# Optimization experiments

Hardware: AMD Instinct MI355X
Metric: run time of the kernel (lower is better)

The kernel has to match this reference:

```python
import jax, jax.numpy as jnp
import numpy as np

N_DOC, SEQ, HID, HEADS = 4, 1024, 768, 12
NE, NM, NP = 48, 4, 1000
L, EMB, BLK, GHID = 97, 768, 64, 500
NEDGE_R = 800


def setup_inputs() -> dict:
    key = jax.random.key(0)
    ks = jax.random.split(key, 24)
    s = 0.02
    att = jax.random.uniform(ks[1], (N_DOC, HEADS, SEQ, SEQ), jnp.float32)
    inp = {
        "sequence_output": jax.random.normal(ks[0], (N_DOC, SEQ, HID), jnp.float32),
        "attention": att / att.sum(-1, keepdims=True),
        "mention_starts": jax.random.randint(ks[2], (N_DOC, NE, NM), 0, SEQ - 2),
        "mention_mask": jnp.ones((N_DOC, NE, NM), jnp.bool_),
        "hts": jax.random.randint(ks[3], (N_DOC, NP, 2), 0, NE),
        "label_emb": jax.random.normal(ks[4], (L, EMB), jnp.float32),
        "gat_W0": jax.random.normal(ks[5], (EMB, 2 * GHID), jnp.float32) * s,
        "gat_al0": jax.random.normal(ks[6], (2, GHID), jnp.float32) * s,
        "gat_ar0": jax.random.normal(ks[7], (2, GHID), jnp.float32) * s,
        "gat_b0": jnp.zeros((2 * GHID,), jnp.float32),
        "gat_W1": jax.random.normal(ks[8], (2 * GHID, EMB), jnp.float32) * s,
        "gat_al1": jax.random.normal(ks[9], (1, EMB), jnp.float32) * s,
        "gat_ar1": jax.random.normal(ks[10], (1, EMB), jnp.float32) * s,
        "gat_b1": jnp.zeros((EMB,), jnp.float32),
        "edge_src": jnp.concatenate([jax.random.randint(ks[11], (NEDGE_R,), 0, L), jnp.arange(L)]),
        "edge_dst": jnp.concatenate([jax.random.randint(ks[12], (NEDGE_R,), 0, L), jnp.arange(L)]),
        "head_W": jax.random.normal(ks[13], (2 * HID, EMB), jnp.float32) * s,
        "head_b": jnp.zeros((EMB,), jnp.float32),
        "tail_W": jax.random.normal(ks[14], (2 * HID, EMB), jnp.float32) * s,
        "tail_b": jnp.zeros((EMB,), jnp.float32),
        "ln_g": jnp.ones((L,), jnp.float32),
        "ln_b": jnp.zeros((L,), jnp.float32),
        "lin2_W": jax.random.normal(ks[15], (2 * L, L), jnp.float32) * s,
        "lin2_b": jnp.zeros((L,), jnp.float32),
        "bil_W": jax.random.normal(ks[16], (EMB * BLK + L, L), jnp.float32) * s,
        "bil_b": jnp.zeros((L,), jnp.float32),
    }
    return inp


def gat_layer(x, W, al, ar, b, src, dst, n_nodes):
    # DGL-style GATConv: per-head linear, additive attention, softmax over incoming edges.
    heads, out_dim = al.shape
    feat = (x @ W).reshape(-1, heads, out_dim)          # [N, H, D]
    el = (feat * al[None]).sum(-1)                      # [N, H]
    er = (feat * ar[None]).sum(-1)
    e = jax.nn.leaky_relu(el[src] + er[dst], 0.2)       # [E, H]
    emax = jax.ops.segment_max(e, dst, num_segments=n_nodes)
    w = jnp.exp(e - emax[dst])
    den = jax.ops.segment_sum(w, dst, num_segments=n_nodes)
    alpha = w / (den[dst] + 1e-9)
    out = jax.ops.segment_sum(alpha[:, :, None] * feat[src], dst, num_segments=n_nodes)
    return out + b.reshape(heads, out_dim)              # [N, H, D]


def reference(sequence_output, attention, mention_starts, mention_mask, hts, label_emb,
              gat_W0, gat_al0, gat_ar0, gat_b0, gat_W1, gat_al1, gat_ar1, gat_b1,
              edge_src, edge_dst, head_W, head_b, tail_W, tail_b,
              ln_g, ln_b, lin2_W, lin2_b, bil_W, bil_b):
    n, c, d = sequence_output.shape
    nl = label_emb.shape[0]
    OFFSET = 1  # bert-style cls offset
    pos = mention_starts + OFFSET                               # [n, E, M], all < c
    bi = jnp.arange(n)[:, None, None]
    m_emb = sequence_output[bi, pos]                            # [n, E, M, d]
    m_att = attention[bi, :, pos]                               # [n, E, M, h, c]
    mf = mention_mask.astype(sequence_output.dtype)
    cnt = mf.sum(2)                                             # [n, E]
    lse = jax.nn.logsumexp(jnp.where(mention_mask[..., None], m_emb, -1e30), axis=2)
    ent_emb = jnp.where(cnt[..., None] > 0, lse, 0.0)           # [n, E, d]
    ent_att = (m_att * mf[..., None, None]).sum(2) / (cnt[..., None, None] + 1e-9)  # [n, E, h, c]
    bi2 = jnp.arange(n)[:, None]
    hidx, tidx = hts[..., 0], hts[..., 1]
    hs = ent_emb[bi2, hidx]                                     # [n, P, d]
    ts = ent_emb[bi2, tidx]
    ht = (ent_att[bi2, hidx] * ent_att[bi2, tidx]).mean(2)      # [n, P, c]
    ht = ht / (ht.sum(-1, keepdims=True) + 1e-5)
    rs = jnp.einsum('npc,ncd->npd', ht, sequence_output)        # [n, P, d]
    hs, ts, rs = hs.reshape(-1, d), ts.reshape(-1, d), rs.reshape(-1, d)
    # GAT over the label co-occurrence graph
    h0 = jax.nn.elu(gat_layer(label_emb, gat_W0, gat_al0, gat_ar0, gat_b0, edge_src, edge_dst, nl))
    h0 = h0.reshape(nl, -1)                                     # concat 2 heads -> [L, 1000]
    lab = gat_layer(h0, gat_W1, gat_al1, gat_ar1, gat_b1, edge_src, edge_dst, nl).mean(1)  # [L, emb]
    def lnorm(x):
        mu = x.mean(-1, keepdims=True)
        v = ((x - mu) ** 2).mean(-1, keepdims=True)
        return (x - mu) / jnp.sqrt(v + 1e-5) * ln_g + ln_b
    hsl = lnorm(hs @ lab.T)
    tsl = lnorm(ts @ lab.T)
    logits_lab = jnp.concatenate([hsl, tsl], 1) @ lin2_W + lin2_b   # [N, L]
    h2 = jnp.tanh(jnp.concatenate([hs, rs], 1) @ head_W + head_b)   # [N, emb]
    t2 = jnp.tanh(jnp.concatenate([ts, rs], 1) @ tail_W + tail_b)
    emb = h2.shape[1]
    b1 = h2.reshape(-1, emb // BLK, BLK)
    b2 = t2.reshape(-1, emb // BLK, BLK)
    bl = (b1[:, :, :, None] * b2[:, :, None, :]).reshape(-1, emb * BLK)  # [N, emb*blk]
    logits = jnp.concatenate([bl, logits_lab], 1) @ bil_W + bil_b        # [N, L]
    return logits
```

## Files before the change

kernel.cpp:

```cpp
#include <hip/hip_runtime.h>
#include <hip/hip_bf16.h>
#include <math.h>

#define NDOC 4
#define SEQL 1024
#define HIDD 768
#define NHEADS 12
#define NEENT 48
#define NMEN 4
#define NPAIR 1000
#define NLAB 97
#define GHID 500
#define NEDGE 897
#define NROW (NDOC*NPAIR)

#define KBIL 49152
#define KSTEPS_MAIN 1536
#define KSTEPS_TOT 1540
#define NPAD 128
#define NPOUT 112
#define NCHUNK 12
#define NMT64 63

#define PB_WPREP 3080
#define PB_SEQ   1536
#define PB_EMB   192
#define PB_ATT   2304

typedef __attribute__((ext_vector_type(8))) short short8v;
typedef __attribute__((ext_vector_type(4))) short short4v;
typedef __attribute__((ext_vector_type(4))) float f32x4;
typedef _Float16 half8v __attribute__((ext_vector_type(8)));
typedef unsigned int uint4v __attribute__((ext_vector_type(4)));

__device__ __forceinline__ unsigned short f2bfbits(float x) {
    return __builtin_bit_cast(unsigned short, __float2bfloat16(x));
}

__device__ __forceinline__ float block_reduce_sum(float v, float* red) {
    int tid = threadIdx.x;
    red[tid] = v;
    __syncthreads();
    for (int s = blockDim.x >> 1; s > 0; s >>= 1) {
        if (tid < s) red[tid] += red[tid + s];
        __syncthreads();
    }
    float r = red[0];
    __syncthreads();
    return r;
}

__device__ __forceinline__ float block_reduce_max(float v, float* red) {
    int tid = threadIdx.x;
    red[tid] = v;
    __syncthreads();
    for (int s = blockDim.x >> 1; s > 0; s >>= 1) {
        if (tid < s) red[tid] = fmaxf(red[tid], red[tid + s]);
        __syncthreads();
    }
    float r = red[0];
    __syncthreads();
    return r;
}

__global__ void __launch_bounds__(256) k_prep_all(
    const float* __restrict__ bil_W, _Float16* __restrict__ Wb,
    const float* __restrict__ seq, __hip_bfloat16* __restrict__ seqb,
    const int* __restrict__ mstarts, float* __restrict__ ent_emb,
    const float* __restrict__ att, float* __restrict__ ent_att)
{
    int bid = blockIdx.x;
    if (bid < PB_WPREP) {
        int t = bid * 256 + threadIdx.x;
        int lane = t & 63;
        int nt = (t >> 6) & 7;
        int kt = t >> 9;
        int col = nt * 16 + (lane & 15);
        int kbase = kt * 32 + ((lane >> 4) << 3);
        half8v v;
        #pragma unroll
        for (int e = 0; e < 8; ++e) {
            int k = kbase + e;
            float x = (col < NLAB && k < (KBIL + NLAB)) ? bil_W[(size_t)k * NLAB + col] : 0.f;
            v[e] = (_Float16)x;
        }
        ((half8v*)Wb)[t] = v;
    } else if (bid < PB_WPREP + PB_SEQ) {
        int t = (bid - PB_WPREP) * 256 + threadIdx.x;
        int lane = t & 63;
        int rest = t >> 6;
        int dt = rest % 48; rest /= 48;
        int kt = rest % 32;
        int doc = rest / 32;
        int d = dt * 16 + (lane & 15);
        int kbase = kt * 32 + ((lane >> 4) << 3);
        short8v v;
        #pragma unroll
        for (int e = 0; e < 8; ++e)
            v[e] = (short)f2bfbits(seq[((size_t)doc * SEQL + kbase + e) * HIDD + d]);
        ((short8v*)seqb)[t] = v;
    } else if (bid < PB_WPREP + PB_SEQ + PB_EMB) {
        int be = bid - (PB_WPREP + PB_SEQ);
        int b = be / NEENT;
        int pos[NMEN];
        #pragma unroll
        for (int m = 0; m < NMEN; ++m) pos[m] = mstarts[be * NMEN + m] + 1;
        for (int d = threadIdx.x; d < HIDD; d += 256) {
            float v0 = seq[((size_t)b * SEQL + pos[0]) * HIDD + d];
            float v1 = seq[((size_t)b * SEQL + pos[1]) * HIDD + d];
            float v2 = seq[((size_t)b * SEQL + pos[2]) * HIDD + d];
            float v3 = seq[((size_t)b * SEQL + pos[3]) * HIDD + d];
            float mx = fmaxf(fmaxf(v0, v1), fmaxf(v2, v3));
            float s = expf(v0 - mx) + expf(v1 - mx) + expf(v2 - mx) + expf(v3 - mx);
            ent_emb[(size_t)be * HIDD + d] = mx + logf(s);
        }
    } else {
        int idx = bid - (PB_WPREP + PB_SEQ + PB_EMB);
        int h = idx % NHEADS;
        int be = idx / NHEADS;
        int b = be / NEENT;
        int pos[NMEN];
        #pragma unroll
        for (int m = 0; m < NMEN; ++m) pos[m] = mstarts[be * NMEN + m] + 1;
        const float* abase = att + ((size_t)b * NHEADS + h) * SEQL * SEQL;
        for (int s = threadIdx.x; s < SEQL; s += 256) {
            float acc = 0.f;
            #pragma unroll
            for (int m = 0; m < NMEN; ++m) acc += abase[(size_t)pos[m] * SEQL + s];
            ent_att[(size_t)idx * SEQL + s] = acc * 0.25f;
        }
    }
}

__global__ void __launch_bounds__(256) k_prep2(
    const float* __restrict__ head_W, __hip_bfloat16* __restrict__ Whb,
    const float* __restrict__ tail_W, __hip_bfloat16* __restrict__ Wtb,
    const float* __restrict__ ent_emb, __hip_bfloat16* __restrict__ emb_bf)
{
    int bid = blockIdx.x;
    if (bid < 1152) {
        const float* W = bid < 576 ? head_W : tail_W;
        __hip_bfloat16* Wf = bid < 576 ? Whb : Wtb;
        int t = (bid % 576) * 256 + threadIdx.x;
        int lane = t & 63;
        int ntile = (t >> 6) % 48;
        int kt = t / (48 * 64);
        int col = ntile * 16 + (lane & 15);
        int kbase = kt * 32 + ((lane >> 4) << 3);
        short8v v;
        #pragma unroll
        for (int e = 0; e < 8; ++e)
            v[e] = (short)f2bfbits(W[(size_t)(kbase + e) * HIDD + col]);
        ((short8v*)Wf)[t] = v;
    } else {
        int t = (bid - 1152) * 256 + threadIdx.x;
        if (t >= NDOC * NEENT * HIDD / 8) return;
        const float4* p = (const float4*)(ent_emb + (size_t)t * 8);
        float4 a = p[0], b = p[1];
        short8v v;
        v[0] = (short)f2bfbits(a.x); v[1] = (short)f2bfbits(a.y);
        v[2] = (short)f2bfbits(a.z); v[3] = (short)f2bfbits(a.w);
        v[4] = (short)f2bfbits(b.x); v[5] = (short)f2bfbits(b.y);
        v[6] = (short)f2bfbits(b.z); v[7] = (short)f2bfbits(b.w);
        ((short8v*)emb_bf)[t] = v;
    }
}

template<int K, int N>
__global__ void __launch_bounds__(256) k_gemm2(
    const float* __restrict__ A, const float* __restrict__ W, float* __restrict__ C)
{
    const int JT = (N + 255) / 256;
    int n  = blockIdx.x / JT;
    int jt = blockIdx.x % JT;
    int j = jt * 256 + threadIdx.x;
    if (j >= N) return;
    const float* a = A + (size_t)n * K;
    float acc0 = 0.f, acc1 = 0.f, acc2 = 0.f, acc3 = 0.f;
    float acc4 = 0.f, acc5 = 0.f, acc6 = 0.f, acc7 = 0.f;
    for (int k = 0; k < K; k += 8) {
        acc0 += a[k + 0] * W[(size_t)(k + 0) * N + j];
        acc1 += a[k + 1] * W[(size_t)(k + 1) * N + j];
        acc2 += a[k + 2] * W[(size_t)(k + 2) * N + j];
        acc3 += a[k + 3] * W[(size_t)(k + 3) * N + j];
        acc4 += a[k + 4] * W[(size_t)(k + 4) * N + j];
        acc5 += a[k + 5] * W[(size_t)(k + 5) * N + j];
        acc6 += a[k + 6] * W[(size_t)(k + 6) * N + j];
        acc7 += a[k + 7] * W[(size_t)(k + 7) * N + j];
    }
    C[(size_t)n * N + j] = ((acc0 + acc1) + (acc2 + acc3)) + ((acc4 + acc5) + (acc6 + acc7));
}

template<int NH, int OD>
__global__ void k_eler(const float* __restrict__ feat, const float* __restrict__ al,
                       const float* __restrict__ ar, float* __restrict__ el,
                       float* __restrict__ er)
{
    __shared__ float red[256];
    int n = blockIdx.x;
    for (int h = 0; h < NH; ++h) {
        float a = 0.f, b = 0.f;
        for (int k = threadIdx.x; k < OD; k += blockDim.x) {
            float f = feat[(size_t)n * NH * OD + h * OD + k];
            a += f * al[h * OD + k];
            b += f * ar[h * OD + k];
        }
        float sa = block_reduce_sum(a, red);
        float sb = block_reduce_sum(b, red);
        if (threadIdx.x == 0) { el[n * NH + h] = sa; er[n * NH + h] = sb; }
    }
}

template<int NH, int OD, int QN, int DO_ELU>
__global__ void k_gat_agg(const float* __restrict__ feat,
                          const float* __restrict__ el, const float* __restrict__ er,
                          const int* __restrict__ esrc, const int* __restrict__ edst,
                          const float* __restrict__ bias, float* __restrict__ out)
{
    __shared__ float red[256];
    __shared__ int ss[NEDGE];
    __shared__ int dd[NEDGE];
    int n = blockIdx.x;
    for (int t = threadIdx.x; t < NEDGE; t += blockDim.x) { ss[t] = esrc[t]; dd[t] = edst[t]; }
    __syncthreads();
    float ern[NH], emax[NH], den[NH];
    #pragma unroll
    for (int h = 0; h < NH; ++h) ern[h] = er[n * NH + h];
    #pragma unroll
    for (int h = 0; h < NH; ++h) {
        float mx = -1e30f;
        for (int t = threadIdx.x; t < NEDGE; t += blockDim.x) {
            if (dd[t] == n) {
                float x = el[ss[t] * NH + h] + ern[h];
                x = x > 0.f ? x : 0.2f * x;
                mx = fmaxf(mx, x);
            }
        }
        emax[h] = block_reduce_max(mx, red);
        float sm = 0.f;
        for (int t = threadIdx.x; t < NEDGE; t += blockDim.x) {
            if (dd[t] == n) {
                float x = el[ss[t] * NH + h] + ern[h];
                x = x > 0.f ? x : 0.2f * x;
                sm += expf(x - emax[h]);
            }
        }
        den[h] = block_reduce_sum(sm, red);
    }
    float acc[QN];
    #pragma unroll
    for (int q = 0; q < QN; ++q) acc[q] = 0.f;
    for (int t = 0; t < NEDGE; ++t) {
        if (dd[t] != n) continue;
        int s = ss[t];
        float alpha[NH];
        #pragma unroll
        for (int h = 0; h < NH; ++h) {
            float x = el[s * NH + h] + ern[h];
            x = x > 0.f ? x : 0.2f * x;
            alpha[h] = expf(x - emax[h]) / (den[h] + 1e-9f);
        }
        #pragma unroll
        for (int q = 0; q < QN; ++q) {
            int idx = threadIdx.x + q * 256;
            if (idx < NH * OD) {
                int h = idx / OD;
                acc[q] += alpha[h] * feat[(size_t)s * NH * OD + idx];
            }
        }
    }
    #pragma unroll
    for (int q = 0; q < QN; ++q) {
        int idx = threadIdx.x + q * 256;
        if (idx < NH * OD) {
            float v = acc[q] + bias[idx];
            out[(size_t)n * NH * OD + idx] = DO_ELU ? (v > 0.f ? v : expm1f(v)) : v;
        }
    }
}

__global__ void k_labtrans(const float* __restrict__ lab, float* __restrict__ labT)
{
    int t = blockIdx.x * 256 + threadIdx.x;
    if (t >= NLAB * HIDD) return;
    int l = t / HIDD, d = t - l * HIDD;
    labT[d * NLAB + l] = lab[t];
}

__global__ void __launch_bounds__(128) k_ent_lab(
    const float* __restrict__ ent_emb, const float* __restrict__ labT,
    const float* __restrict__ ln_g, const float* __restrict__ ln_b,
    float* __restrict__ EL)
{
    __shared__ float e[HIDD];
    __shared__ float red[128];
    int be = blockIdx.x;
    for (int k = threadIdx.x; k < HIDD; k += 128) e[k] = ent_emb[(size_t)be * HIDD + k];
    __syncthreads();
    int l = threadIdx.x;
    float a = 0.f;
    if (l < NLAB)
        for (int k = 0; k < HIDD; ++k) a += e[k] * labT[k * NLAB + l];
    float v = (l < NLAB) ? a : 0.f;
    float s  = block_reduce_sum(v, red);
    float s2 = block_reduce_sum(v * v, red);
    const float invL = 1.0f / NLAB;
    float mu = s * invL;
    float var = s2 * invL - mu * mu;
    float is = 1.0f / sqrtf(var + 1e-5f);
    if (l < NLAB) EL[be * NLAB + l] = (a - mu) * is * ln_g[l] + ln_b[l];
}

__global__ void __launch_bounds__(128) k_lin2(
    const float* __restrict__ EL, const int* __restrict__ hts,
    const float* __restrict__ lin2_W, const float* __restrict__ lin2_b,
    _Float16* __restrict__ llhf)
{
    __shared__ float sh[NLAB], st[NLAB];
    int n = blockIdx.x;
    int b = n / NPAIR;
    int hi = hts[n * 2], ti = hts[n * 2 + 1];
    int l = threadIdx.x;
    if (l < NLAB) {
        sh[l] = EL[(b * NEENT + hi) * NLAB + l];
        st[l] = EL[(b * NEENT + ti) * NLAB + l];
    }
    __syncthreads();
    float a = 0.f;
    if (l < NLAB) {
        a = lin2_b[l];
        for (int q = 0; q < NLAB; ++q)
            a += sh[q] * lin2_W[q * NLAB + l] + st[q] * lin2_W[(NLAB + q) * NLAB + l];
    }
    llhf[(size_t)n * NPAD + l] = (_Float16)(l < NLAB ? a : 0.f);
}

__global__ void __launch_bounds__(256) k_ht(
    const float* __restrict__ ent_att, const int* __restrict__ hts,
    __hip_bfloat16* __restrict__ HTb)
{
    __shared__ float red[256];
    int n = blockIdx.x;
    n = (n & 7) * 500 + (n >> 3);
    int b = n / NPAIR;
    int hi = hts[n * 2], ti = hts[n * 2 + 1];
    const float* ha = ent_att + ((size_t)(b * NEENT + hi)) * NHEADS * SEQL;
    const float* ta = ent_att + ((size_t)(b * NEENT + ti)) * NHEADS * SEQL;
    int s0 = threadIdx.x * 4;
    float4 acc = {0.f, 0.f, 0.f, 0.f};
    #pragma unroll
    for (int h = 0; h < NHEADS; ++h) {
        float4 a = *(const float4*)&ha[h * SEQL + s0];
        float4 t = *(const float4*)&ta[h * SEQL + s0];
        acc.x += a.x * t.x; acc.y += a.y * t.y; acc.z += a.z * t.z; acc.w += a.w * t.w;
    }
    const float inv12 = 1.0f / NHEADS;
    acc.x *= inv12; acc.y *= inv12; acc.z *= inv12; acc.w *= inv12;
    float Z = block_reduce_sum(acc.x + acc.y + acc.z + acc.w, red);
    float scale = 1.0f / (Z + 1e-5f);
    int nloc = n % NPAIR;
    short4v v;
    v.x = (short)f2bfbits(acc.x * scale);
    v.y = (short)f2bfbits(acc.y * scale);
    v.z = (short)f2bfbits(acc.z * scale);
    v.w = (short)f2bfbits(acc.w * scale);
    *(short4v*)&HTb[((size_t)b * 1024 + nloc) * SEQL + s0] = v;
}

__global__ void __launch_bounds__(256) k_rs_mfma(
    const __hip_bfloat16* __restrict__ HTb, const __hip_bfloat16* __restrict__ seqb,
    __hip_bfloat16* __restrict__ rsb)
{
    int b = blockIdx.x;
    int wg = (b & 7) * 96 + (b >> 3);
    int doc = wg / 192;
    int rem = wg % 192;
    int mtile = rem / 6, ngrp = rem % 6;
    int tid = threadIdx.x, wave = tid >> 6, lane = tid & 63;
    int mh = wave & 1, ng = wave >> 1;
    int lr = lane & 15, lg = lane >> 4;
    int rowl = mtile * 32 + mh * 16 + lr;
    const short8v* av = (const short8v*)(HTb + (((size_t)doc * 1024 + rowl) * SEQL));
    const short8v* bv = (const short8v*)seqb;
    int dtbase = ngrp * 8 + ng * 4;
    f32x4 acc[4];
    #pragma unroll
    for (int nt = 0; nt < 4; ++nt) acc[nt] = f32x4{0.f, 0.f, 0.f, 0.f};
    for (int kt = 0; kt < 32; ++kt) {
        short8v af = av[kt * 4 + lg];
        const short8v* wp = bv + ((((size_t)doc * 32 + kt) * 48 + dtbase) * 64 + lane);
        #pragma unroll
        for (int nt = 0; nt < 4; ++nt)
            acc[nt] = __builtin_amdgcn_mfma_f32_16x16x32_bf16(af, wp[nt * 64], acc[nt], 0, 0, 0);
    }
    #pragma unroll
    for (int nt = 0; nt < 4; ++nt) {
        int d = ngrp * 128 + ng * 64 + nt * 16 + lr;
        #pragma unroll
        for (int r = 0; r < 4; ++r) {
            int nloc = mtile * 32 + mh * 16 + lg * 4 + r;
            if (nloc < NPAIR)
                rsb[((size_t)(doc * NPAIR + nloc)) * HIDD + d] = __float2bfloat16(acc[nt][r]);
        }
    }
}

__global__ void __launch_bounds__(256) k_ht2_mfma(
    const __hip_bfloat16* __restrict__ emb_bf, const __hip_bfloat16* __restrict__ rsb,
    const int* __restrict__ hts,
    const __hip_bfloat16* __restrict__ Whb, const __hip_bfloat16* __restrict__ Wtb,
    const float* __restrict__ head_b, const float* __restrict__ tail_b,
    float* __restrict__ h2, float* __restrict__ t2)
{
    int bid = blockIdx.x;
    int which = bid >= (NMT64 * 6) ? 1 : 0;
    int rem = bid - which * (NMT64 * 6);
    int mtile = rem / 6, ngrp = rem % 6;
    int tid = threadIdx.x, wave = tid >> 6, lane = tid & 63;
    int ng = wave & 1, mp = wave >> 1;
    int lr = lane & 15, lg = lane >> 4;
    int na = mtile * 64 + mp * 32 + lr;
    int nb = na + 16;
    int nac = na < NROW ? na : NROW - 1;
    int nbc = nb < NROW ? nb : NROW - 1;
    int ba = nac / NPAIR, bb = nbc / NPAIR;
    int enta = hts[nac * 2 + which];
    int entb = hts[nbc * 2 + which];
    const short8v* embrow_a = (const short8v*)emb_bf + (size_t)(ba * NEENT + enta) * 96;
    const short8v* embrow_b = (const short8v*)emb_bf + (size_t)(bb * NEENT + entb) * 96;
    const short8v* rsrow_a  = (const short8v*)rsb + (size_t)nac * 96;
    const short8v* rsrow_b  = (const short8v*)rsb + (size_t)nbc * 96;
    const short8v* wv = (const short8v*)(which ? Wtb : Whb);
    const float* bias = which ? tail_b : head_b;
    float* out = which ? t2 : h2;
    f32x4 acc[2][4];
    #pragma unroll
    for (int m = 0; m < 2; ++m)
        #pragma unroll
        for (int nt = 0; nt < 4; ++nt) acc[m][nt] = f32x4{0.f, 0.f, 0.f, 0.f};
    int ntbase = ngrp * 8 + ng * 4;
    for (int kt = 0; kt < 24; ++kt) {
        short8v afa = embrow_a[kt * 4 + lg];
        short8v afb = embrow_b[kt * 4 + lg];
        const short8v* wp = wv + ((kt * 48 + ntbase) * 64 + lane);
        #pragma unroll
        for (int nt = 0; nt < 4; ++nt) {
            short8v bf = wp[nt * 64];
            acc[0][nt] = __builtin_amdgcn_mfma_f32_16x16x32_bf16(afa, bf, acc[0][nt], 0, 0, 0);
            acc[1][nt] = __builtin_amdgcn_mfma_f32_16x16x32_bf16(afb, bf, acc[1][nt], 0, 0, 0);
        }
    }
    for (int kt = 24; kt < 48; ++kt) {
        short8v afa = rsrow_a[(kt - 24) * 4 + lg];
        short8v afb = rsrow_b[(kt - 24) * 4 + lg];
        const short8v* wp = wv + ((kt * 48 + ntbase) * 64 + lane);
        #pragma unroll
        for (int nt = 0; nt < 4; ++nt) {
            short8v bf = wp[nt * 64];
            acc[0][nt] = __builtin_amdgcn_mfma_f32_16x16x32_bf16(afa, bf, acc[0][nt], 0, 0, 0);
            acc[1][nt] = __builtin_amdgcn_mfma_f32_16x16x32_bf16(afb, bf, acc[1][nt], 0, 0, 0);
        }
    }
    #pragma unroll
    for (int m = 0; m < 2; ++m) {
        #pragma unroll
        for (int nt = 0; nt < 4; ++nt) {
            int col = ngrp * 128 + ng * 64 + nt * 16 + lr;
            float bj = bias[col];
            #pragma unroll
            for (int r = 0; r < 4; ++r) {
                int n2 = mtile * 64 + mp * 32 + m * 16 + lg * 4 + r;
                if (n2 < NROW)
                    out[(size_t)n2 * HIDD + col] = tanhf(acc[m][nt][r] + bj);
            }
        }
    }
}

__global__ void __launch_bounds__(256) k_bilin_mfma(
    const float* __restrict__ h2, const float* __restrict__ t2,
    const _Float16* __restrict__ llhf, const _Float16* __restrict__ Wb,
    float* __restrict__ pout)
{
    __shared__ unsigned int hs2[64 * 68];
    __shared__ _Float16 ts[64 * 72];
    int bid = blockIdx.x;
    int c = bid % NCHUNK;
    int mtile = bid / NCHUNK;
    int n0 = mtile * 64;
    int tid = threadIdx.x;
    int wave = tid >> 6, lane = tid & 63;
    int ng = wave & 1, mp = wave >> 1;
    int lr = lane & 15;
    int lg = lane >> 4;
    int koff = lg << 3;
    int rowa = mp * 32 + lr;
    int rowb = rowa + 16;
    f32x4 acc[2][4];
    #pragma unroll
    for (int m = 0; m < 2; ++m)
        #pragma unroll
        for (int nt = 0; nt < 4; ++nt) acc[m][nt] = f32x4{0.f, 0.f, 0.f, 0.f};

    const half8v* wbv = (const half8v*)Wb;

    for (int idx = tid; idx < 4096; idx += 256) {
        int r = idx >> 6, cc = idx & 63;
        float hv = h2[(size_t)(n0 + r) * HIDD + c * 64 + cc];
        float tv = t2[(size_t)(n0 + r) * HIDD + c * 64 + cc];
        unsigned short hb = __builtin_bit_cast(unsigned short, (_Float16)hv);
        hs2[r * 68 + cc] = ((unsigned int)hb << 16) | hb;
        ts[r * 72 + cc] = (_Float16)tv;
    }
    __syncthreads();
    for (int j0 = 0; j0 < 64; j0 += 32) {
        half8v tva = *(const half8v*)&ts[rowa * 72 + j0 + koff];
        half8v tvb = *(const half8v*)&ts[rowb * 72 + j0 + koff];
        int ktbase = c * 128 + (j0 >> 5);
        #pragma unroll 4
        for (int i = 0; i < 64; ++i) {
            unsigned int ha = hs2[rowa * 68 + i];
            unsigned int hb = hs2[rowb * 68 + i];
            half8v afa = __builtin_bit_cast(half8v, uint4v{ha, ha, ha, ha}) * tva;
            half8v afb = __builtin_bit_cast(half8v, uint4v{hb, hb, hb, hb}) * tvb;
            int kt = ktbase + i * 2;
            const half8v* wp = wbv + ((kt * 8 + ng * 4) * 64 + lane);
            #pragma unroll
            for (int nt = 0; nt < 4; ++nt) {
                half8v bf = wp[nt * 64];
                acc[0][nt] = __builtin_amdgcn_mfma_f32_16x16x32_f16(afa, bf, acc[0][nt], 0, 0, 0);
                acc[1][nt] = __builtin_amdgcn_mfma_f32_16x16x32_f16(afb, bf, acc[1][nt], 0, 0, 0);
            }
        }
    }
    if (c == NCHUNK - 1) {
        const half8v* lv = (const half8v*)llhf;
        #pragma unroll
        for (int tt = 0; tt < 4; ++tt) {
            half8v afa = lv[(size_t)(n0 + rowa) * 16 + tt * 4 + lg];
            half8v afb = lv[(size_t)(n0 + rowb) * 16 + tt * 4 + lg];
            int kt = KSTEPS_MAIN + tt;
            const half8v* wp = wbv + ((kt * 8 + ng * 4) * 64 + lane);
            #pragma unroll
            for (int nt = 0; nt < 4; ++nt) {
                half8v bf = wp[nt * 64];
                acc[0][nt] = __builtin_amdgcn_mfma_f32_16x16x32_f16(afa, bf, acc[0][nt], 0, 0, 0);
                acc[1][nt] = __builtin_amdgcn_mfma_f32_16x16x32_f16(afb, bf, acc[1][nt], 0, 0, 0);
            }
        }
    }
    #pragma unroll
    for (int m = 0; m < 2; ++m) {
        #pragma unroll
        for (int nt = 0; nt < 4; ++nt) {
            int col = ng * 64 + nt * 16 + lr;
            if (col < NPOUT) {
                #pragma unroll
                for (int r = 0; r < 4; ++r) {
                    int rown = n0 + mp * 32 + m * 16 + lg * 4 + r;
                    if (rown < NROW)
                        pout[((size_t)c * NROW + rown) * NPOUT + col] = acc[m][nt][r];
                }
            }
        }
    }
}

__global__ void k_bilin_reduce(const float* __restrict__ pout,
                               const float* __restrict__ bil_b,
                               float* __restrict__ out)
{
    int t = blockIdx.x * 256 + threadIdx.x;
    if (t >= NROW * NLAB) return;
    int n = t / NLAB, l = t - n * NLAB;
    float a = bil_b[l];
    #pragma unroll
    for (int q = 0; q < NCHUNK; ++q) a += pout[((size_t)q * NROW + n) * NPOUT + l];
    out[t] = a;
}

extern "C" void kernel_launch(void* const* d_in, const int* in_sizes, int n_in,
                              void* d_out, int out_size, void* d_ws, size_t ws_size,
                              hipStream_t stream)
{
    (void)in_sizes; (void)n_in; (void)out_size; (void)ws_size;
    const float* seq       = (const float*)d_in[0];
    const float* att       = (const float*)d_in[1];
    const int*   mstarts   = (const int*)d_in[2];
    const int*   hts       = (const int*)d_in[4];
    const float* label_emb = (const float*)d_in[5];
    const float* gat_W0    = (const float*)d_in[6];
    const float* gat_al0   = (const float*)d_in[7];
    const float* gat_ar0   = (const float*)d_in[8];
    const float* gat_b0    = (const float*)d_in[9];
    const float* gat_W1    = (const float*)d_in[10];
    const float* gat_al1   = (const float*)d_in[11];
    const float* gat_ar1   = (const float*)d_in[12];
    const float* gat_b1    = (const float*)d_in[13];
    const int*   esrc      = (const int*)d_in[14];
    const int*   edst      = (const int*)d_in[15];
    const float* head_W    = (const float*)d_in[16];
    const float* head_b    = (const float*)d_in[17];
    const float* tail_W    = (const float*)d_in[18];
    const float* tail_b    = (const float*)d_in[19];
    const float* ln_g      = (const float*)d_in[20];
    const float* ln_b      = (const float*)d_in[21];
    const float* lin2_W    = (const float*)d_in[22];
    const float* lin2_b    = (const float*)d_in[23];
    const float* bil_W     = (const float*)d_in[24];
    const float* bil_b     = (const float*)d_in[25];
    float* out = (float*)d_out;
    float* ws  = (float*)d_ws;

    float* ent_emb    = ws;
    float* ent_att    = ws + 147456;
    float* rs_region  = ws + 2506752;
    float* h2         = ws + 5578752;
    float* t2         = ws + 8650752;
    float* EL         = ws + 11722752;
    float* labT       = ws + 11741376;
    float* feat0      = ws + 12110752;
    float* el0        = ws + 12207752;
    float* er0        = ws + 12207952;
    float* h0         = ws + 12208152;
    float* feat1      = ws + 12305152;
    float* el1        = ws + 12379648;
    float* er1        = ws + 12379752;
    float* lab        = ws + 12379856;
    _Float16* llhf    = (_Float16*)(ws + 12454352);
    _Float16* Wb      = (_Float16*)(ws + 12710352);
    __hip_bfloat16* Whb    = (__hip_bfloat16*)(ws + 147456);
    __hip_bfloat16* Wtb    = (__hip_bfloat16*)(ws + 147456 + 589824);
    __hip_bfloat16* emb_bf = (__hip_bfloat16*)(ws + 147456 + 1179648);
    float* pout = ws + 147456;
    __hip_bfloat16* HTb  = (__hip_bfloat16*)h2;
    __hip_bfloat16* seqb = (__hip_bfloat16*)t2;
    __hip_bfloat16* rsb  = (__hip_bfloat16*)rs_region;

    k_prep_all<<<PB_WPREP + PB_SEQ + PB_EMB + PB_ATT, 256, 0, stream>>>(
        bil_W, Wb, seq, seqb, mstarts, ent_emb, att, ent_att);

    k_gemm2<768, 1000><<<NLAB * 4, 256, 0, stream>>>(label_emb, gat_W0, feat0);
    k_eler<2, 500><<<NLAB, 256, 0, stream>>>(feat0, gat_al0, gat_ar0, el0, er0);
    k_gat_agg<2, 500, 4, 1><<<NLAB, 256, 0, stream>>>(feat0, el0, er0, esrc, edst, gat_b0, h0);
    k_gemm2<1000, 768><<<NLAB * 3, 256, 0, stream>>>(h0, gat_W1, feat1);
    k_eler<1, 768><<<NLAB, 256, 0, stream>>>(feat1, gat_al1, gat_ar1, el1, er1);
    k_gat_agg<1, 768, 3, 0><<<NLAB, 256, 0, stream>>>(feat1, el1, er1, esrc, edst, gat_b1, lab);

    k_labtrans<<<(NLAB * HIDD + 255) / 256, 256, 0, stream>>>(lab, labT);
    k_ent_lab<<<NDOC * NEENT, 128, 0, stream>>>(ent_emb, labT, ln_g, ln_b, EL);
    k_lin2<<<NROW, 128, 0, stream>>>(EL, hts, lin2_W, lin2_b, llhf);

    k_ht<<<NROW, 256, 0, stream>>>(ent_att, hts, HTb);

    k_prep2<<<1224, 256, 0, stream>>>(head_W, Whb, tail_W, Wtb, ent_emb, emb_bf);

    k_rs_mfma<<<768, 256, 0, stream>>>(HTb, seqb, rsb);

    k_ht2_mfma<<<2 * NMT64 * 6, 256, 0, stream>>>(emb_bf, rsb, hts, Whb, Wtb, head_b, tail_b, h2, t2);

    k_bilin_mfma<<<NMT64 * NCHUNK, 256, 0, stream>>>(h2, t2, llhf, Wb, pout);
    k_bilin_reduce<<<(NROW * NLAB + 255) / 256, 256, 0, stream>>>(pout, bil_b, out);
}
```

Baseline: 470.4 us.

## Fuse prep kernels, prefetch MFMA operands, split bilinear chunks finer

Folds the first GAT GEMM and the head/tail weight conversion into the big prep kernel. It merges the label transpose into the GAT aggregation and the entity bf16 conversion into k_ht, which removes several launches. The rs and ht2 MFMA loops now load the next k-step's operands one iteration ahead (software prefetch), and the bilinear kernel splits each chunk into two j-halves (NCHUNK 24), giving more blocks and a smaller LDS footprint. The workspace is re-laid out so buffers no longer alias, and the cost is a larger pout and twice as many partials to reduce.

```diff
diff --git a/kernel.cpp b/kernel.cpp
--- a/kernel.cpp
+++ b/kernel.cpp
@@ -19,13 +19,16 @@
 #define KSTEPS_TOT 1540
 #define NPAD 128
 #define NPOUT 112
-#define NCHUNK 12
+#define NCHUNK 24
 #define NMT64 63
 
+#define PB_G0    388
 #define PB_WPREP 3080
 #define PB_SEQ   1536
 #define PB_EMB   192
 #define PB_ATT   2304
+#define PB_WHT   1152
+#define PB_TOT   (PB_G0+PB_WPREP+PB_SEQ+PB_EMB+PB_ATT+PB_WHT)
 
 typedef __attribute__((ext_vector_type(8))) short short8v;
 typedef __attribute__((ext_vector_type(4))) short short4v;
@@ -64,12 +67,37 @@
 }
 
 __global__ void __launch_bounds__(256) k_prep_all(
+    const float* __restrict__ label_emb, const float* __restrict__ gat_W0,
+    float* __restrict__ feat0,
     const float* __restrict__ bil_W, _Float16* __restrict__ Wb,
     const float* __restrict__ seq, __hip_bfloat16* __restrict__ seqb,
     const int* __restrict__ mstarts, float* __restrict__ ent_emb,
-    const float* __restrict__ att, float* __restrict__ ent_att)
+    const float* __restrict__ att, float* __restrict__ ent_att,
+    const float* __restrict__ head_W, __hip_bfloat16* __restrict__ Whb,
+    const float* __restrict__ tail_W, __hip_bfloat16* __restrict__ Wtb)
 {
     int bid = blockIdx.x;
+    if (bid < PB_G0) {
+        int n = bid >> 2, jt = bid & 3;
+        int j = jt * 256 + threadIdx.x;
+        if (j < 1000) {
+            const float* a = label_emb + (size_t)n * 768;
+            float a0=0.f,a1=0.f,a2=0.f,a3=0.f,a4=0.f,a5=0.f,a6=0.f,a7=0.f;
+            for (int k = 0; k < 768; k += 8) {
+                a0 += a[k+0] * gat_W0[(size_t)(k+0)*1000 + j];
+                a1 += a[k+1] * gat_W0[(size_t)(k+1)*1000 + j];
+                a2 += a[k+2] * gat_W0[(size_t)(k+2)*1000 + j];
+                a3 += a[k+3] * gat_W0[(size_t)(k+3)*1000 + j];
+                a4 += a[k+4] * gat_W0[(size_t)(k+4)*1000 + j];
+                a5 += a[k+5] * gat_W0[(size_t)(k+5)*1000 + j];
+                a6 += a[k+6] * gat_W0[(size_t)(k+6)*1000 + j];
+                a7 += a[k+7] * gat_W0[(size_t)(k+7)*1000 + j];
+            }
+            feat0[(size_t)n*1000 + j] = ((a0+a1)+(a2+a3))+((a4+a5)+(a6+a7));
+        }
+        return;
+    }
+    bid -= PB_G0;
     if (bid < PB_WPREP) {
         int t = bid * 256 + threadIdx.x;
         int lane = t & 63;
@@ -85,8 +113,11 @@
             v[e] = (_Float16)x;
         }
         ((half8v*)Wb)[t] = v;
-    } else if (bid < PB_WPREP + PB_SEQ) {
-        int t = (bid - PB_WPREP) * 256 + threadIdx.x;
+        return;
+    }
+    bid -= PB_WPREP;
+    if (bid < PB_SEQ) {
+        int t = bid * 256 + threadIdx.x;
         int lane = t & 63;
         int rest = t >> 6;
         int dt = rest % 48; rest /= 48;
@@ -99,8 +130,11 @@
         for (int e = 0; e < 8; ++e)
             v[e] = (short)f2bfbits(seq[((size_t)doc * SEQL + kbase + e) * HIDD + d]);
         ((short8v*)seqb)[t] = v;
-    } else if (bid < PB_WPREP + PB_SEQ + PB_EMB) {
-        int be = bid - (PB_WPREP + PB_SEQ);
+        return;
+    }
+    bid -= PB_SEQ;
+    if (bid < PB_EMB) {
+        int be = bid;
         int b = be / NEENT;
         int pos[NMEN];
         #pragma unroll
@@ -114,8 +148,11 @@
             float s = expf(v0 - mx) + expf(v1 - mx) + expf(v2 - mx) + expf(v3 - mx);
             ent_emb[(size_t)be * HIDD + d] = mx + logf(s);
         }
-    } else {
-        int idx = bid - (PB_WPREP + PB_SEQ + PB_EMB);
+        return;
+    }
+    bid -= PB_EMB;
+    if (bid < PB_ATT) {
+        int idx = bid;
         int h = idx % NHEADS;
         int be = idx / NHEADS;
         int b = be / NEENT;
@@ -129,16 +166,10 @@
             for (int m = 0; m < NMEN; ++m) acc += abase[(size_t)pos[m] * SEQL + s];
             ent_att[(size_t)idx * SEQL + s] = acc * 0.25f;
         }
-    }
-}
-
-__global__ void __launch_bounds__(256) k_prep2(
-    const float* __restrict__ head_W, __hip_bfloat16* __restrict__ Whb,
-    const float* __restrict__ tail_W, __hip_bfloat16* __restrict__ Wtb,
-    const float* __restrict__ ent_emb, __hip_bfloat16* __restrict__ emb_bf)
-{
-    int bid = blockIdx.x;
-    if (bid < 1152) {
+        return;
+    }
+    bid -= PB_ATT;
+    {
         const float* W = bid < 576 ? head_W : tail_W;
         __hip_bfloat16* Wf = bid < 576 ? Whb : Wtb;
         int t = (bid % 576) * 256 + threadIdx.x;
@@ -152,17 +183,6 @@
         for (int e = 0; e < 8; ++e)
             v[e] = (short)f2bfbits(W[(size_t)(kbase + e) * HIDD + col]);
         ((short8v*)Wf)[t] = v;
-    } else {
-        int t = (bid - 1152) * 256 + threadIdx.x;
-        if (t >= NDOC * NEENT * HIDD / 8) return;
-        const float4* p = (const float4*)(ent_emb + (size_t)t * 8);
-        float4 a = p[0], b = p[1];
-        short8v v;
-        v[0] = (short)f2bfbits(a.x); v[1] = (short)f2bfbits(a.y);
-        v[2] = (short)f2bfbits(a.z); v[3] = (short)f2bfbits(a.w);
-        v[4] = (short)f2bfbits(b.x); v[5] = (short)f2bfbits(b.y);
-        v[6] = (short)f2bfbits(b.z); v[7] = (short)f2bfbits(b.w);
-        ((short8v*)emb_bf)[t] = v;
     }
 }
 
@@ -211,11 +231,12 @@
     }
 }
 
-template<int NH, int OD, int QN, int DO_ELU>
+template<int NH, int OD, int QN, int DO_ELU, int WLT>
 __global__ void k_gat_agg(const float* __restrict__ feat,
                           const float* __restrict__ el, const float* __restrict__ er,
                           const int* __restrict__ esrc, const int* __restrict__ edst,
-                          const float* __restrict__ bias, float* __restrict__ out)
+                          const float* __restrict__ bias, float* __restrict__ out,
+                          float* __restrict__ labT)
 {
     __shared__ float red[256];
     __shared__ int ss[NEDGE];
@@ -274,17 +295,11 @@
         int idx = threadIdx.x + q * 256;
         if (idx < NH * OD) {
             float v = acc[q] + bias[idx];
-            out[(size_t)n * NH * OD + idx] = DO_ELU ? (v > 0.f ? v : expm1f(v)) : v;
-        }
-    }
-}
-
-__global__ void k_labtrans(const float* __restrict__ lab, float* __restrict__ labT)
-{
-    int t = blockIdx.x * 256 + threadIdx.x;
-    if (t >= NLAB * HIDD) return;
-    int l = t / HIDD, d = t - l * HIDD;
-    labT[d * NLAB + l] = lab[t];
+            float o = DO_ELU ? (v > 0.f ? v : expm1f(v)) : v;
+            out[(size_t)n * NH * OD + idx] = o;
+            if (WLT) labT[(size_t)idx * NLAB + n] = o;
+        }
+    }
 }
 
 __global__ void __launch_bounds__(128) k_ent_lab(
@@ -337,11 +352,24 @@
 
 __global__ void __launch_bounds__(256) k_ht(
     const float* __restrict__ ent_att, const int* __restrict__ hts,
-    __hip_bfloat16* __restrict__ HTb)
+    __hip_bfloat16* __restrict__ HTb,
+    const float* __restrict__ ent_emb, __hip_bfloat16* __restrict__ emb_bf)
 {
     __shared__ float red[256];
-    int n = blockIdx.x;
-    n = (n & 7) * 500 + (n >> 3);
+    int bid = blockIdx.x;
+    if (bid >= NROW) {
+        int t = (bid - NROW) * 256 + threadIdx.x;
+        const float4* p = (const float4*)(ent_emb + (size_t)t * 8);
+        float4 a = p[0], b = p[1];
+        short8v v;
+        v[0] = (short)f2bfbits(a.x); v[1] = (short)f2bfbits(a.y);
+        v[2] = (short)f2bfbits(a.z); v[3] = (short)f2bfbits(a.w);
+        v[4] = (short)f2bfbits(b.x); v[5] = (short)f2bfbits(b.y);
+        v[6] = (short)f2bfbits(b.z); v[7] = (short)f2bfbits(b.w);
+        ((short8v*)emb_bf)[t] = v;
+        return;
+    }
+    int n = (bid & 7) * 500 + (bid >> 3);
     int b = n / NPAIR;
     int hi = hts[n * 2], ti = hts[n * 2 + 1];
     const float* ha = ent_att + ((size_t)(b * NEENT + hi)) * NHEADS * SEQL;
@@ -386,12 +414,24 @@
     f32x4 acc[4];
     #pragma unroll
     for (int nt = 0; nt < 4; ++nt) acc[nt] = f32x4{0.f, 0.f, 0.f, 0.f};
+    const short8v* wp0 = bv + ((((size_t)doc * 32) * 48 + dtbase) * 64 + lane);
+    short8v bc[4];
+    #pragma unroll
+    for (int nt = 0; nt < 4; ++nt) bc[nt] = wp0[nt * 64];
+    short8v ac = av[lg];
     for (int kt = 0; kt < 32; ++kt) {
-        short8v af = av[kt * 4 + lg];
-        const short8v* wp = bv + ((((size_t)doc * 32 + kt) * 48 + dtbase) * 64 + lane);
+        int ktn = kt < 31 ? kt + 1 : 31;
+        const short8v* wpn = bv + ((((size_t)doc * 32 + ktn) * 48 + dtbase) * 64 + lane);
+        short8v bn[4];
+        #pragma unroll
+        for (int nt = 0; nt < 4; ++nt) bn[nt] = wpn[nt * 64];
+        short8v an = av[ktn * 4 + lg];
         #pragma unroll
         for (int nt = 0; nt < 4; ++nt)
-            acc[nt] = __builtin_amdgcn_mfma_f32_16x16x32_bf16(af, wp[nt * 64], acc[nt], 0, 0, 0);
+            acc[nt] = __builtin_amdgcn_mfma_f32_16x16x32_bf16(ac, bc[nt], acc[nt], 0, 0, 0);
+        ac = an;
+        #pragma unroll
+        for (int nt = 0; nt < 4; ++nt) bc[nt] = bn[nt];
     }
     #pragma unroll
     for (int nt = 0; nt < 4; ++nt) {
@@ -439,27 +479,29 @@
         #pragma unroll
         for (int nt = 0; nt < 4; ++nt) acc[m][nt] = f32x4{0.f, 0.f, 0.f, 0.f};
     int ntbase = ngrp * 8 + ng * 4;
-    for (int kt = 0; kt < 24; ++kt) {
-        short8v afa = embrow_a[kt * 4 + lg];
-        short8v afb = embrow_b[kt * 4 + lg];
-        const short8v* wp = wv + ((kt * 48 + ntbase) * 64 + lane);
+    short8v aca = embrow_a[lg], acb = embrow_b[lg];
+    const short8v* wp0 = wv + ((size_t)(0 * 48 + ntbase) * 64 + lane);
+    short8v bc[4];
+    #pragma unroll
+    for (int nt = 0; nt < 4; ++nt) bc[nt] = wp0[nt * 64];
+    for (int kt = 0; kt < 48; ++kt) {
+        int ktn = kt < 47 ? kt + 1 : 47;
+        const short8v* pa = ktn < 24 ? embrow_a + ktn * 4 : rsrow_a + (ktn - 24) * 4;
+        const short8v* pb = ktn < 24 ? embrow_b + ktn * 4 : rsrow_b + (ktn - 24) * 4;
+        short8v ana = pa[lg];
+        short8v anb = pb[lg];
+        const short8v* wpn = wv + (((size_t)ktn * 48 + ntbase) * 64 + lane);
+        short8v bn[4];
+        #pragma unroll
+        for (int nt = 0; nt < 4; ++nt) bn[nt] = wpn[nt * 64];
         #pragma unroll
         for (int nt = 0; nt < 4; ++nt) {
-            short8v bf = wp[nt * 64];
-            acc[0][nt] = __builtin_amdgcn_mfma_f32_16x16x32_bf16(afa, bf, acc[0][nt], 0, 0, 0);
-            acc[1][nt] = __builtin_amdgcn_mfma_f32_16x16x32_bf16(afb, bf, acc[1][nt], 0, 0, 0);
-        }
-    }
-    for (int kt = 24; kt < 48; ++kt) {
-        short8v afa = rsrow_a[(kt - 24) * 4 + lg];
-        short8v afb = rsrow_b[(kt - 24) * 4 + lg];
-        const short8v* wp = wv + ((kt * 48 + ntbase) * 64 + lane);
-        #pragma unroll
-        for (int nt = 0; nt < 4; ++nt) {
-            short8v bf = wp[nt * 64];
-            acc[0][nt] = __builtin_amdgcn_mfma_f32_16x16x32_bf16(afa, bf, acc[0][nt], 0, 0, 0);
-            acc[1][nt] = __builtin_amdgcn_mfma_f32_16x16x32_bf16(afb, bf, acc[1][nt], 0, 0, 0);
-        }
+            acc[0][nt] = __builtin_amdgcn_mfma_f32_16x16x32_bf16(aca, bc[nt], acc[0][nt], 0, 0, 0);
+            acc[1][nt] = __builtin_amdgcn_mfma_f32_16x16x32_bf16(acb, bc[nt], acc[1][nt], 0, 0, 0);
+        }
+        aca = ana; acb = anb;
+        #pragma unroll
+        for (int nt = 0; nt < 4; ++nt) bc[nt] = bn[nt];
     }
     #pragma unroll
     for (int m = 0; m < 2; ++m) {
@@ -483,10 +525,13 @@
     float* __restrict__ pout)
 {
     __shared__ unsigned int hs2[64 * 68];
-    __shared__ _Float16 ts[64 * 72];
+    __shared__ _Float16 ts[64 * 40];
     int bid = blockIdx.x;
-    int c = bid % NCHUNK;
+    int chunk = bid % NCHUNK;
     int mtile = bid / NCHUNK;
+    int c  = chunk >> 1;
+    int jh = chunk & 1;
+    int j0 = jh * 32;
     int n0 = mtile * 64;
     int tid = threadIdx.x;
     int wave = tid >> 6, lane = tid & 63;
@@ -507,40 +552,49 @@
     for (int idx = tid; idx < 4096; idx += 256) {
         int r = idx >> 6, cc = idx & 63;
         float hv = h2[(size_t)(n0 + r) * HIDD + c * 64 + cc];
-        float tv = t2[(size_t)(n0 + r) * HIDD + c * 64 + cc];
         unsigned short hb = __builtin_bit_cast(unsigned short, (_Float16)hv);
         hs2[r * 68 + cc] = ((unsigned int)hb << 16) | hb;
-        ts[r * 72 + cc] = (_Float16)tv;
+    }
+    for (int idx = tid; idx < 2048; idx += 256) {
+        int r = idx >> 5, cc = idx & 31;
+        ts[r * 40 + cc] = (_Float16)t2[(size_t)(n0 + r) * HIDD + c * 64 + j0 + cc];
     }
     __syncthreads();
-    for (int j0 = 0; j0 < 64; j0 += 32) {
-        half8v tva = *(const half8v*)&ts[rowa * 72 + j0 + koff];
-        half8v tvb = *(const half8v*)&ts[rowb * 72 + j0 + koff];
-        int ktbase = c * 128 + (j0 >> 5);
-        #pragma unroll 4
-        for (int i = 0; i < 64; ++i) {
-            unsigned int ha = hs2[rowa * 68 + i];
-            unsigned int hb = hs2[rowb * 68 + i];
-            half8v afa = __builtin_bit_cast(half8v, uint4v{ha, ha, ha, ha}) * tva;
-            half8v afb = __builtin_bit_cast(half8v, uint4v{hb, hb, hb, hb}) * tvb;
-            int kt = ktbase + i * 2;
-            const half8v* wp = wbv + ((kt * 8 + ng * 4) * 64 + lane);
-            #pragma unroll
-            for (int nt = 0; nt < 4; ++nt) {
-                half8v bf = wp[nt * 64];
-                acc[0][nt] = __builtin_amdgcn_mfma_f32_16x16x32_f16(afa, bf, acc[0][nt], 0, 0, 0);
-                acc[1][nt] = __builtin_amdgcn_mfma_f32_16x16x32_f16(afb, bf, acc[1][nt], 0, 0, 0);
-            }
-        }
-    }
-    if (c == NCHUNK - 1) {
+
+    half8v tva = *(const half8v*)&ts[rowa * 40 + koff];
+    half8v tvb = *(const half8v*)&ts[rowb * 40 + koff];
+    int ktbase = c * 128 + jh;
+    const half8v* wpb = wbv + (((size_t)ktbase * 8 + ng * 4) * 64 + lane);
+    half8v bc[4];
+    #pragma unroll
+    for (int nt = 0; nt < 4; ++nt) bc[nt] = wpb[nt * 64];
+    #pragma unroll 4
+    for (int i = 0; i < 64; ++i) {
+        int in = i < 63 ? i + 1 : 63;
+        const half8v* wpn = wpb + (size_t)in * 1024;
+        half8v bn[4];
+        #pragma unroll
+        for (int nt = 0; nt < 4; ++nt) bn[nt] = wpn[nt * 64];
+        unsigned int ha = hs2[rowa * 68 + i];
+        unsigned int hb = hs2[rowb * 68 + i];
+        half8v afa = __builtin_bit_cast(half8v, uint4v{ha, ha, ha, ha}) * tva;
+        half8v afb = __builtin_bit_cast(half8v, uint4v{hb, hb, hb, hb}) * tvb;
+        #pragma unroll
+        for (int nt = 0; nt < 4; ++nt) {
+            acc[0][nt] = __builtin_amdgcn_mfma_f32_16x16x32_f16(afa, bc[nt], acc[0][nt], 0, 0, 0);
+            acc[1][nt] = __builtin_amdgcn_mfma_f32_16x16x32_f16(afb, bc[nt], acc[1][nt], 0, 0, 0);
+        }
+        #pragma unroll
+        for (int nt = 0; nt < 4; ++nt) bc[nt] = bn[nt];
+    }
+    if (chunk == NCHUNK - 1) {
         const half8v* lv = (const half8v*)llhf;
         #pragma unroll
         for (int tt = 0; tt < 4; ++tt) {
             half8v afa = lv[(size_t)(n0 + rowa) * 16 + tt * 4 + lg];
             half8v afb = lv[(size_t)(n0 + rowb) * 16 + tt * 4 + lg];
             int kt = KSTEPS_MAIN + tt;
-            const half8v* wp = wbv + ((kt * 8 + ng * 4) * 64 + lane);
+            const half8v* wp = wbv + (((size_t)kt * 8 + ng * 4) * 64 + lane);
             #pragma unroll
             for (int nt = 0; nt < 4; ++nt) {
                 half8v bf = wp[nt * 64];
@@ -559,7 +613,7 @@
                 for (int r = 0; r < 4; ++r) {
                     int rown = n0 + mp * 32 + m * 16 + lg * 4 + r;
                     if (rown < NROW)
-                        pout[((size_t)c * NROW + rown) * NPOUT + col] = acc[m][nt][r];
+                        pout[((size_t)chunk * NROW + rown) * NPOUT + col] = acc[m][nt][r];
                 }
             }
         }
@@ -610,50 +664,47 @@
     const float* bil_W     = (const float*)d_in[24];
     const float* bil_b     = (const float*)d_in[25];
     float* out = (float*)d_out;
-    float* ws  = (float*)d_ws;
-
-    float* ent_emb    = ws;
-    float* ent_att    = ws + 147456;
-    float* rs_region  = ws + 2506752;
-    float* h2         = ws + 5578752;
-    float* t2         = ws + 8650752;
-    float* EL         = ws + 11722752;
-    float* labT       = ws + 11741376;
-    float* feat0      = ws + 12110752;
-    float* el0        = ws + 12207752;
-    float* er0        = ws + 12207952;
-    float* h0         = ws + 12208152;
-    float* feat1      = ws + 12305152;
-    float* el1        = ws + 12379648;
-    float* er1        = ws + 12379752;
-    float* lab        = ws + 12379856;
-    _Float16* llhf    = (_Float16*)(ws + 12454352);
-    _Float16* Wb      = (_Float16*)(ws + 12710352);
-    __hip_bfloat16* Whb    = (__hip_bfloat16*)(ws + 147456);
-    __hip_bfloat16* Wtb    = (__hip_bfloat16*)(ws + 147456 + 589824);
-    __hip_bfloat16* emb_bf = (__hip_bfloat16*)(ws + 147456 + 1179648);
-    float* pout = ws + 147456;
-    __hip_bfloat16* HTb  = (__hip_bfloat16*)h2;
-    __hip_bfloat16* seqb = (__hip_bfloat16*)t2;
-    __hip_bfloat16* rsb  = (__hip_bfloat16*)rs_region;
-
-    k_prep_all<<<PB_WPREP + PB_SEQ + PB_EMB + PB_ATT, 256, 0, stream>>>(
-        bil_W, Wb, seq, seqb, mstarts, ent_emb, att, ent_att);
-
-    k_gemm2<768, 1000><<<NLAB * 4, 256, 0, stream>>>(label_emb, gat_W0, feat0);
+
+    float* p = (float*)d_ws;
+    auto alloc = [&](size_t n) { float* r = p; p += ((n + 15) & ~(size_t)15); return r; };
+    float* ent_emb = alloc(147456);
+    float* ent_att = alloc(2359296);
+    float* EL      = alloc(18624);
+    float* labT    = alloc(74496);
+    float* feat0   = alloc(97000);
+    float* el0     = alloc(200);
+    float* er0     = alloc(200);
+    float* h0      = alloc(97000);
+    float* feat1   = alloc(74496);
+    float* el1     = alloc(104);
+    float* er1     = alloc(104);
+    float* lab     = alloc(74496);
+    float* h2      = alloc((size_t)4096 * 768);
+    float* t2      = alloc((size_t)4096 * 768);
+    float* pout    = alloc((size_t)NCHUNK * NROW * NPOUT);
+    __hip_bfloat16* HTb    = (__hip_bfloat16*)alloc(2097152);
+    __hip_bfloat16* seqb   = (__hip_bfloat16*)alloc(1572864);
+    __hip_bfloat16* rsb    = (__hip_bfloat16*)alloc(1536000);
+    __hip_bfloat16* Whb    = (__hip_bfloat16*)alloc(589824);
+    __hip_bfloat16* Wtb    = (__hip_bfloat16*)alloc(589824);
+    __hip_bfloat16* emb_bf = (__hip_bfloat16*)alloc(73728);
+    _Float16* llhf = (_Float16*)alloc(262144);
+    _Float16* Wb   = (_Float16*)alloc(3153920);
+
+    k_prep_all<<<PB_TOT, 256, 0, stream>>>(
+        label_emb, gat_W0, feat0, bil_W, Wb, seq, seqb, mstarts, ent_emb,
+        att, ent_att, head_W, Whb, tail_W, Wtb);
+
     k_eler<2, 500><<<NLAB, 256, 0, stream>>>(feat0, gat_al0, gat_ar0, el0, er0);
-    k_gat_agg<2, 500, 4, 1><<<NLAB, 256, 0, stream>>>(feat0, el0, er0, esrc, edst, gat_b0, h0);
+    k_gat_agg<2, 500, 4, 1, 0><<<NLAB, 256, 0, stream>>>(feat0, el0, er0, esrc, edst, gat_b0, h0, nullptr);
     k_gemm2<1000, 768><<<NLAB * 3, 256, 0, stream>>>(h0, gat_W1, feat1);
     k_eler<1, 768><<<NLAB, 256, 0, stream>>>(feat1, gat_al1, gat_ar1, el1, er1);
-    k_gat_agg<1, 768, 3, 0><<<NLAB, 256, 0, stream>>>(feat1, el1, er1, esrc, edst, gat_b1, lab);
-
-    k_labtrans<<<(NLAB * HIDD + 255) / 256, 256, 0, stream>>>(lab, labT);
+    k_gat_agg<1, 768, 3, 0, 1><<<NLAB, 256, 0, stream>>>(feat1, el1, er1, esrc, edst, gat_b1, lab, labT);
+
     k_ent_lab<<<NDOC * NEENT, 128, 0, stream>>>(ent_emb, labT, ln_g, ln_b, EL);
     k_lin2<<<NROW, 128, 0, stream>>>(EL, hts, lin2_W, lin2_b, llhf);
 
-    k_ht<<<NROW, 256, 0, stream>>>(ent_att, hts, HTb);
-
-    k_prep2<<<1224, 256, 0, stream>>>(head_W, Whb, tail_W, Wtb, ent_emb, emb_bf);
+    k_ht<<<NROW + 72, 256, 0, stream>>>(ent_att, hts, HTb, ent_emb, emb_bf);
 
     k_rs_mfma<<<768, 256, 0, stream>>>(HTb, seqb, rsb);
 
```

Measured after the change: 455.2 us. 1.03x faster.
